# Kernel optimization log

Measured on AMD Instinct MI355X. Metric: run time of the kernel, lower is better.

Reference implementation:

```python
import jax, jax.numpy as jnp
import numpy as np
import math

B, S, D, H, DFF = 16, 512, 1024, 16, 4096
DK = D // H
EPS = 1e-6


def _lin(x, W, b):
    return x @ W + b


def _layernorm(x, g, b):
    # torch-style: unbiased std, eps added to std (not var)
    m = jnp.mean(x, axis=-1, keepdims=True)
    std = jnp.sqrt(jnp.sum((x - m) ** 2, axis=-1, keepdims=True) / (x.shape[-1] - 1))
    return g * (x - m) / (std + EPS) + b


def _gelu(x):
    return 0.5 * x * (1.0 + jnp.tanh(jnp.sqrt(2.0 / jnp.pi) * (x + 0.044715 * x ** 3)))


def setup_inputs() -> dict:
    key = jax.random.key(0)
    ks = jax.random.split(key, 20)
    sc = lambda fan_in: 1.0 / math.sqrt(fan_in)
    d = {
        "x": jax.random.normal(ks[0], (B, S, D), jnp.float32),
        "time": jax.random.normal(ks[1], (B, S, D), jnp.float32),
        "Wq": jax.random.uniform(ks[2], (D, D), jnp.float32, -sc(D), sc(D)),
        "bq": jnp.zeros((D,), jnp.float32),
        "Wk": jax.random.uniform(ks[3], (D, D), jnp.float32, -sc(D), sc(D)),
        "bk": jnp.zeros((D,), jnp.float32),
        "Wt": jax.random.uniform(ks[4], (D, D), jnp.float32, -sc(D), sc(D)),
        "bt": jnp.zeros((D,), jnp.float32),
        "Wv": jax.random.uniform(ks[5], (D, D), jnp.float32, -sc(D), sc(D)),
        "bv": jnp.zeros((D,), jnp.float32),
        "Wo": jax.random.uniform(ks[6], (D, D), jnp.float32, -sc(D), sc(D)),
        "bo": jnp.zeros((D,), jnp.float32),
        "W1": jax.random.uniform(ks[7], (D, DFF), jnp.float32, -sc(D), sc(D)),
        "b1": jnp.zeros((DFF,), jnp.float32),
        "W2": jax.random.uniform(ks[8], (DFF, D), jnp.float32, -sc(DFF), sc(DFF)),
        "b2": jnp.zeros((D,), jnp.float32),
        "ln1_g": jnp.ones((D,), jnp.float32),
        "ln1_b": jnp.zeros((D,), jnp.float32),
        "ln2_g": jnp.ones((D,), jnp.float32),
        "ln2_b": jnp.zeros((D,), jnp.float32),
        "mask_logits": jax.random.uniform(ks[9], (S, S), jnp.float32, 2.0, 5.0),
        "mask": jax.random.randint(ks[10], (B, 1, S, S), 0, 2, jnp.int32),
        "pmask": 0,
    }
    return d


def reference(x, time, Wq, bq, Wk, bk, Wt, bt, Wv, bv, Wo, bo, W1, b1, W2, b2,
              ln1_g, ln1_b, ln2_g, ln2_b, mask_logits, mask, pmask):
    def split_heads(t):  # [B,S,D] -> [B,H,S,DK]
        return t.reshape(B, S, H, DK).transpose(0, 2, 1, 3)

    # --- attention sublayer (dropout = identity at inference) ---
    xn = _layernorm(x, ln1_g, ln1_b)
    q = split_heads(_lin(xn, Wq, bq))
    k1 = split_heads(_lin(xn, Wk, bk))
    k2 = split_heads(_lin(time, Wt, bt))
    v = split_heads(_lin(xn, Wv, bv))

    inv = 1.0 / math.sqrt(DK)
    scores = jnp.einsum("bhqd,bhkd->bhqk", q, k1) * inv
    scores = jnp.where(mask == 0, -1e9, scores)  # masked_fill BEFORE time term
    scores = scores + jnp.einsum("bhqd,bhkd->bhqk", q, k2) * inv
    p_attn = jax.nn.softmax(scores, axis=-1)
    p_attn = p_attn * jax.nn.sigmoid(mask_logits)  # learned post-softmax mask [S,S]
    ctx = jnp.einsum("bhqk,bhkd->bhqd", p_attn, v)
    ctx = ctx.transpose(0, 2, 1, 3).reshape(B, S, D)
    x = x + _lin(ctx, Wo, bo)

    # --- FFN sublayer ---
    xn2 = _layernorm(x, ln2_g, ln2_b)
    ff = _lin(_gelu(_lin(xn2, W1, b1)), W2, b2)
    return x + ff
```

## Files before the change

### kernel.cpp

```cpp
#include <hip/hip_runtime.h>

#define BB   16
#define SS   512
#define DD   1024
#define HH   16
#define DKK  64
#define DFFN 4096
#define LN_EPS 1e-6f
#define QSCALE 0.18033688011112042f

typedef __attribute__((ext_vector_type(8))) __bf16 bf16x8;
typedef __attribute__((ext_vector_type(4))) float f32x4;
typedef __attribute__((ext_vector_type(8))) unsigned short ushort8;
typedef __attribute__((ext_vector_type(4))) unsigned short ushort4_t;

#define AS1 __attribute__((address_space(1)))
#define AS3 __attribute__((address_space(3)))

__device__ __forceinline__ unsigned short f2bf(float f) {
  unsigned int u = __float_as_uint(f);
  u += 0x7FFFu + ((u >> 16) & 1u);
  return (unsigned short)(u >> 16);
}
__device__ __forceinline__ float bf2f(unsigned short u) {
  return __uint_as_float(((unsigned int)u) << 16);
}

__device__ __forceinline__ float gelu_f(float x) {
  float x3 = x * x * x;
  return 0.5f * x * (1.0f + tanhf(0.7978845608028654f * (x + 0.044715f * x3)));
}

__device__ __forceinline__ void sbar() {
  __builtin_amdgcn_sched_barrier(0);
  __builtin_amdgcn_s_barrier();
  __builtin_amdgcn_sched_barrier(0);
}
#define WAITVM(N)                                         \
  do {                                                    \
    __builtin_amdgcn_sched_barrier(0);                    \
    asm volatile("s_waitcnt vmcnt(" #N ")" ::: "memory"); \
    __builtin_amdgcn_sched_barrier(0);                    \
  } while (0)

__global__ __launch_bounds__(256) void ln_kernel(const float* __restrict__ x,
                                                 const float* __restrict__ g,
                                                 const float* __restrict__ b,
                                                 unsigned short* __restrict__ out, int ldo) {
  const int row = blockIdx.x;
  const int tid = threadIdx.x;
  const float* xr = x + (size_t)row * DD;
  float4 v = *(const float4*)(xr + tid * 4);
  float s = v.x + v.y + v.z + v.w;
#pragma unroll
  for (int off = 1; off < 64; off <<= 1) s += __shfl_xor(s, off);
  __shared__ float red[8];
  const int wid = tid >> 6, l = tid & 63;
  if (l == 0) red[wid] = s;
  __syncthreads();
  const float mean = (red[0] + red[1] + red[2] + red[3]) * (1.0f / DD);
  float4 d;
  d.x = v.x - mean; d.y = v.y - mean; d.z = v.z - mean; d.w = v.w - mean;
  float ss = d.x * d.x + d.y * d.y + d.z * d.z + d.w * d.w;
#pragma unroll
  for (int off = 1; off < 64; off <<= 1) ss += __shfl_xor(ss, off);
  if (l == 0) red[4 + wid] = ss;
  __syncthreads();
  const float var = (red[4] + red[5] + red[6] + red[7]) * (1.0f / (DD - 1));
  const float scale = 1.0f / (sqrtf(var) + LN_EPS);
  float4 gv = *(const float4*)(g + tid * 4);
  float4 bv = *(const float4*)(b + tid * 4);
  ushort4_t o;
  o[0] = f2bf(gv.x * d.x * scale + bv.x);
  o[1] = f2bf(gv.y * d.y * scale + bv.y);
  o[2] = f2bf(gv.z * d.z * scale + bv.z);
  o[3] = f2bf(gv.w * d.w * scale + bv.w);
  *(ushort4_t*)(out + (size_t)row * ldo + tid * 4) = o;
}

__global__ __launch_bounds__(256) void cvt_bf16(const float* __restrict__ in,
                                                unsigned short* __restrict__ out, int ldo) {
  const int i = blockIdx.x * 256 + threadIdx.x;
  const int row = i >> 7;
  const int c0 = (i & 127) * 8;
  const float4* p = (const float4*)(in + (size_t)row * DD + c0);
  float4 a = p[0], b = p[1];
  ushort8 o;
  o[0] = f2bf(a.x); o[1] = f2bf(a.y); o[2] = f2bf(a.z); o[3] = f2bf(a.w);
  o[4] = f2bf(b.x); o[5] = f2bf(b.y); o[6] = f2bf(b.z); o[7] = f2bf(b.w);
  *(ushort8*)(out + (size_t)row * ldo + c0) = o;
}

__global__ __launch_bounds__(256) void transpose_cvt(const float* __restrict__ W,
                                                     unsigned short* __restrict__ WT,
                                                     int N, int ldo) {
  __shared__ float tile[32][33];
  const int tx = threadIdx.x & 31, ty = threadIdx.x >> 5;
  const int n0 = blockIdx.x * 32, k0 = blockIdx.y * 32;
#pragma unroll
  for (int i = 0; i < 32; i += 8)
    tile[ty + i][tx] = W[(size_t)(k0 + ty + i) * N + n0 + tx];
  __syncthreads();
#pragma unroll
  for (int i = 0; i < 32; i += 8)
    WT[(size_t)(n0 + ty + i) * ldo + k0 + tx] = f2bf(tile[tx][ty + i]);
}

__global__ __launch_bounds__(256) void vtrans(const unsigned short* __restrict__ in,
                                              unsigned short* __restrict__ out) {
  __shared__ unsigned short tile[64][72];
  const int t = threadIdx.x;
  const int c0 = blockIdx.x * 64;
  const int r0 = blockIdx.y * 64;
  const int tx = t & 15, ty = t >> 4;
#pragma unroll
  for (int i = 0; i < 64; i += 16)
    *(ushort4_t*)&tile[ty + i][tx * 4] =
        *(const ushort4_t*)(in + (size_t)(r0 + ty + i) * 1024 + c0 + tx * 4);
  __syncthreads();
  const int cT = t >> 2, rq = (t & 3) * 16;
  ushort8 o0, o1;
#pragma unroll
  for (int j = 0; j < 8; ++j) o0[j] = tile[rq + j][cT];
#pragma unroll
  for (int j = 0; j < 8; ++j) o1[j] = tile[rq + 8 + j][cT];
  *(ushort8*)(out + (size_t)(c0 + cT) * 8192 + r0 + rq) = o0;
  *(ushort8*)(out + (size_t)(c0 + cT) * 8192 + r0 + rq + 8) = o1;
}

__global__ __launch_bounds__(256) void bias_prep(const float* __restrict__ bq,
                                                 const float* __restrict__ bv,
                                                 const float* __restrict__ bk,
                                                 const float* __restrict__ bt,
                                                 float* __restrict__ qvb,
                                                 float* __restrict__ kcb) {
  const int i = blockIdx.x * 256 + threadIdx.x;
  if (i < 2048) qvb[i] = (i < 1024) ? bq[i] : bv[i - 1024];
  else kcb[i - 2048] = bk[i - 2048] + bt[i - 2048];
}

__global__ __launch_bounds__(256) void gate_build(const int* __restrict__ mask,
                                                  const float* __restrict__ ml,
                                                  unsigned short* __restrict__ gate) {
  const int i = blockIdx.x * 256 + threadIdx.x;
  const size_t base = (size_t)i * 8;
  const int off = (int)(base & (SS * SS - 1));
  const int4* mp = (const int4*)(mask + base);
  const int4 m0 = mp[0], m1 = mp[1];
  const float4* lp = (const float4*)(ml + off);
  const float4 a = lp[0], b = lp[1];
  ushort8 o;
  o[0] = m0.x ? f2bf(1.0f / (1.0f + __expf(-a.x))) : 0;
  o[1] = m0.y ? f2bf(1.0f / (1.0f + __expf(-a.y))) : 0;
  o[2] = m0.z ? f2bf(1.0f / (1.0f + __expf(-a.z))) : 0;
  o[3] = m0.w ? f2bf(1.0f / (1.0f + __expf(-a.w))) : 0;
  o[4] = m1.x ? f2bf(1.0f / (1.0f + __expf(-b.x))) : 0;
  o[5] = m1.y ? f2bf(1.0f / (1.0f + __expf(-b.y))) : 0;
  o[6] = m1.z ? f2bf(1.0f / (1.0f + __expf(-b.z))) : 0;
  o[7] = m1.w ? f2bf(1.0f / (1.0f + __expf(-b.w))) : 0;
  *(ushort8*)(gate + base) = o;
}

template <int BM, int EPI>
__global__ __launch_bounds__(512, 2) void gemm8p(const unsigned short* __restrict__ A, int lda,
                                                 const unsigned short* __restrict__ BT,
                                                 const float* __restrict__ bias,
                                                 const float* __restrict__ resid,
                                                 void* __restrict__ Cout,
                                                 unsigned short* __restrict__ vOut,
                                                 int M, int N, int K) {
  constexpr int MI = BM / 32;
  constexpr int ASUB = BM / 16;
  constexpr int AHALF = BM * 32;
  constexpr int ABUF = BM * 64;
  constexpr int ACALL = BM / 128;

  __shared__ __align__(16) unsigned short smA[2 * ABUF];
  __shared__ __align__(16) unsigned short smB[2 * 16384];

  const int tid = threadIdx.x;
  const int w = tid >> 6, lane = tid & 63;
  const int lr = lane & 15, lg = lane >> 4;
  const int wr = w >> 2, wn = w & 3;

  const int nb = N / 256;
  const int nwg = gridDim.x;
  int bid = blockIdx.x;
  bid = (bid & 7) * (nwg >> 3) + (bid >> 3);
  const int mb = bid / nb, nbk = bid % nb;

  const int uo = (lane * 16) ^ (lane & 32);
  const int srow = uo >> 6;
  const int scol = (uo & 63) >> 1;

  const unsigned short* pA[2];
  const unsigned short* pB[2];
#pragma unroll
  for (int j = 0; j < ACALL; ++j)
    pA[j] = A + (size_t)(mb * BM + (j * 8 + w) * 16 + srow) * lda + scol;
  if (ACALL == 1) pA[1] = pA[0];
#pragma unroll
  for (int j = 0; j < 2; ++j)
    pB[j] = BT + (size_t)(nbk * 256 + (j * 8 + w) * 16 + srow) * K + scol;

  auto stA = [&](int kt, int ks, int j, int d) {
    __builtin_amdgcn_global_load_lds(
        (const AS1 void*)(pA[j] + (size_t)kt * 64 + ks * 32),
        (AS3 void*)(smA + d * ABUF + ks * AHALF + j * 4096 + w * 512), 16, 0, 0);
  };
  auto stB = [&](int kt, int ks, int j, int d) {
    __builtin_amdgcn_global_load_lds(
        (const AS1 void*)(pB[j] + (size_t)kt * 64 + ks * 32),
        (AS3 void*)(smB + d * 16384 + ks * 8192 + j * 4096 + w * 512), 16, 0, 0);
  };
  auto issue_half = [&](int t, int ks) {
    const int d = t & 1;
#pragma unroll
    for (int j = 0; j < ACALL; ++j) stA(t, ks, j, d);
    stB(t, ks, 0, d);
    stB(t, ks, 1, d);
  };

  const int aoff = lr * 32 + ((lg * 8) ^ ((lr & 8) << 1));

  f32x4 acc[MI][4] = {};
  const int NT = K >> 6;

  issue_half(0, 0);
  issue_half(0, 1);
  issue_half(1, 0);
  if constexpr (ACALL == 2) { WAITVM(8); } else { WAITVM(6); }
  sbar();

  for (int kt = 0; kt < NT; ++kt) {
    const unsigned short* aD = smA + (kt & 1) * ABUF;
    const unsigned short* bD = smB + (kt & 1) * 16384;
    const bool i1 = (kt + 1 < NT);
    const bool i2 = (kt + 2 < NT);
    bf16x8 af[4], bf[4];

#pragma unroll
    for (int i = 0; i < 4; ++i)
      bf[i] = *(const bf16x8*)(bD + (wn * 4 + i) * 512 + aoff);
#pragma unroll
    for (int i = 0; i < 4; ++i)
      af[i] = *(const bf16x8*)(aD + (wr * MI + i) * 512 + aoff);
    if (i1) issue_half(kt + 1, 1);
    if constexpr (ACALL == 1) {
      if (i1) { WAITVM(6); } else { WAITVM(0); }
    }
    sbar();
    __builtin_amdgcn_s_setprio(1);
#pragma unroll
    for (int mi = 0; mi < 4; ++mi)
#pragma unroll
      for (int ni = 0; ni < 4; ++ni)
        acc[mi][ni] = __builtin_amdgcn_mfma_f32_16x16x32_bf16(af[mi], bf[ni], acc[mi][ni], 0, 0, 0);
    __builtin_amdgcn_s_setprio(0);
    sbar();

    if constexpr (ACALL == 2) {
#pragma unroll
      for (int i = 0; i < 4; ++i)
        af[i] = *(const bf16x8*)(aD + (wr * MI + 4 + i) * 512 + aoff);
      if (i1) { WAITVM(8); } else { WAITVM(0); }
      sbar();
      __builtin_amdgcn_s_setprio(1);
#pragma unroll
      for (int mi = 0; mi < 4; ++mi)
#pragma unroll
        for (int ni = 0; ni < 4; ++ni)
          acc[4 + mi][ni] = __builtin_amdgcn_mfma_f32_16x16x32_bf16(af[mi], bf[ni], acc[4 + mi][ni], 0, 0, 0);
      __builtin_amdgcn_s_setprio(0);
      sbar();
    }

#pragma unroll
    for (int i = 0; i < 4; ++i)
      bf[i] = *(const bf16x8*)(bD + (16 + wn * 4 + i) * 512 + aoff);
#pragma unroll
    for (int i = 0; i < 4; ++i)
      af[i] = *(const bf16x8*)(aD + (ASUB + wr * MI + i) * 512 + aoff);
    if (i2) issue_half(kt + 2, 0);
    if constexpr (ACALL == 1) {
      if (i2) { WAITVM(6); } else { WAITVM(3); }
    }
    sbar();
    __builtin_amdgcn_s_setprio(1);
#pragma unroll
    for (int mi = 0; mi < 4; ++mi)
#pragma unroll
      for (int ni = 0; ni < 4; ++ni)
        acc[mi][ni] = __builtin_amdgcn_mfma_f32_16x16x32_bf16(af[mi], bf[ni], acc[mi][ni], 0, 0, 0);
    __builtin_amdgcn_s_setprio(0);
    sbar();

    if constexpr (ACALL == 2) {
#pragma unroll
      for (int i = 0; i < 4; ++i)
        af[i] = *(const bf16x8*)(aD + (ASUB + wr * MI + 4 + i) * 512 + aoff);
      if (i2) { WAITVM(8); } else { WAITVM(4); }
      sbar();
      __builtin_amdgcn_s_setprio(1);
#pragma unroll
      for (int mi = 0; mi < 4; ++mi)
#pragma unroll
        for (int ni = 0; ni < 4; ++ni)
          acc[4 + mi][ni] = __builtin_amdgcn_mfma_f32_16x16x32_bf16(af[mi], bf[ni], acc[4 + mi][ni], 0, 0, 0);
      __builtin_amdgcn_s_setprio(0);
      sbar();
    }
  }

  const int colb = nbk * 256 + wn * 64;
  const int rowb = mb * BM + wr * (BM / 2);
  float bvv[4];
#pragma unroll
  for (int ni = 0; ni < 4; ++ni) bvv[ni] = bias[colb + ni * 16 + lr];

  if (EPI == 3 && colb >= 1024) {
#pragma unroll
    for (int mi = 0; mi < MI; ++mi) {
#pragma unroll
      for (int j = 0; j < 4; ++j) {
        const int row = rowb + mi * 16 + lg * 4 + j;
#pragma unroll
        for (int ni = 0; ni < 4; ++ni)
          vOut[(size_t)row * 1024 + (colb - 1024) + ni * 16 + lr] = f2bf(acc[mi][ni][j] + bvv[ni]);
      }
    }
  } else {
#pragma unroll
    for (int mi = 0; mi < MI; ++mi) {
#pragma unroll
      for (int j = 0; j < 4; ++j) {
        const int row = rowb + mi * 16 + lg * 4 + j;
#pragma unroll
        for (int ni = 0; ni < 4; ++ni) {
          const int col = colb + ni * 16 + lr;
          float vv = acc[mi][ni][j] + bvv[ni];
          if (EPI == 2) vv = gelu_f(vv);
          if (EPI == 1) {
            const size_t o = (size_t)row * N + col;
            ((float*)Cout)[o] = vv + resid[o];
          } else if (EPI == 3) {
            ((unsigned short*)Cout)[(size_t)row * 1024 + col] = f2bf(vv * QSCALE);
          } else {
            ((unsigned short*)Cout)[(size_t)row * N + col] = f2bf(vv);
          }
        }
      }
    }
  }
}

__global__ __launch_bounds__(256) void attn4(const unsigned short* __restrict__ qb,
                                             const unsigned short* __restrict__ vT,
                                             const unsigned short* __restrict__ kcb,
                                             const unsigned short* __restrict__ gate,
                                             unsigned short* __restrict__ ctx) {
  __shared__ __align__(16) unsigned char smem[33280];
  float* pctx = (float*)smem;
  float* sumw = (float*)(smem + 32768);

  const int tid = threadIdx.x;
  const int w = tid >> 6, l = tid & 63;
  const int lr = l & 15, lg = l >> 4;
  const int virt = (blockIdx.x & 7) * 512 + (blockIdx.x >> 3);
  const int qt = virt & 15;
  const int h = (virt >> 4) & 15;
  const int b = virt >> 8;
  const int q0 = qt * 32;

  const unsigned short* qg = qb + (size_t)b * SS * DD + h * DKK;
  const unsigned short* kg = kcb + (size_t)b * SS * DD + h * DKK;
  const unsigned short* vg = vT + (size_t)(h * DKK) * 8192 + b * SS;
  const unsigned short* gg = gate + (size_t)b * SS * SS;
  unsigned short* cg = ctx + (size_t)b * SS * DD + h * DKK;

  bf16x8 qf[2][2];
#pragma unroll
  for (int mi = 0; mi < 2; ++mi)
#pragma unroll
    for (int ks = 0; ks < 2; ++ks)
      qf[mi][ks] = *(const bf16x8*)(qg + (size_t)(q0 + mi * 16 + lr) * DD + ks * 32 + lg * 8);

  f32x4 acc[2][4] = {};
  float ssum[2][4] = {};
  const int kb0 = w * 128;

#pragma unroll
  for (int it = 0; it < 4; ++it) {
    const int kbase = kb0 + it * 32;
    unsigned short* Pb = (unsigned short*)smem + w * 2560 + (it & 1) * 1280;

    bf16x8 kf[2][2];
#pragma unroll
    for (int ni = 0; ni < 2; ++ni)
#pragma unroll
      for (int ks = 0; ks < 2; ++ks)
        kf[ni][ks] = *(const bf16x8*)(kg + (size_t)(kbase + ni * 16 + lr) * DD + ks * 32 + lg * 8);
    f32x4 sc[2][2] = {};
#pragma unroll
    for (int ks = 0; ks < 2; ++ks)
#pragma unroll
      for (int mi = 0; mi < 2; ++mi)
#pragma unroll
        for (int ni = 0; ni < 2; ++ni)
          sc[mi][ni] = __builtin_amdgcn_mfma_f32_16x16x32_bf16(qf[mi][ks], kf[ni][ks], sc[mi][ni], 0, 0, 0);

    bf16x8 vb[4];
#pragma unroll
    for (int dkg = 0; dkg < 4; ++dkg)
      vb[dkg] = *(const bf16x8*)(vg + (size_t)(dkg * 16 + lr) * 8192 + kbase + lg * 8);

#pragma unroll
    for (int mi = 0; mi < 2; ++mi)
#pragma unroll
      for (int ni = 0; ni < 2; ++ni)
#pragma unroll
        for (int j = 0; j < 4; ++j) {
          const int row = mi * 16 + lg * 4 + j;
          const unsigned short gu = gg[(size_t)(q0 + row) * SS + kbase + ni * 16 + lr];
          const float e = exp2f(sc[mi][ni][j]);
          ssum[mi][j] += gu ? e : 0.0f;
          Pb[row * 40 + ni * 16 + lr] = f2bf(e * bf2f(gu));
        }

#pragma unroll
    for (int mi = 0; mi < 2; ++mi) {
      const bf16x8 pa = *(const bf16x8*)(Pb + (mi * 16 + lr) * 40 + lg * 8);
#pragma unroll
      for (int dkg = 0; dkg < 4; ++dkg)
        acc[mi][dkg] = __builtin_amdgcn_mfma_f32_16x16x32_bf16(pa, vb[dkg], acc[mi][dkg], 0, 0, 0);
    }
  }

#pragma unroll
  for (int mi = 0; mi < 2; ++mi)
#pragma unroll
    for (int j = 0; j < 4; ++j) {
      float s = ssum[mi][j];
      s += __shfl_xor(s, 1);
      s += __shfl_xor(s, 2);
      s += __shfl_xor(s, 4);
      s += __shfl_xor(s, 8);
      if (lr == 0) sumw[w * 32 + mi * 16 + lg * 4 + j] = s;
    }
  __syncthreads();

#pragma unroll
  for (int mi = 0; mi < 2; ++mi)
#pragma unroll
    for (int dkg = 0; dkg < 4; ++dkg)
#pragma unroll
      for (int j = 0; j < 4; ++j)
        pctx[(size_t)w * 2048 + (mi * 16 + lg * 4 + j) * 64 + dkg * 16 + lr] = acc[mi][dkg][j];
  __syncthreads();

  {
    const int row = tid >> 3;
    const int dk0 = (tid & 7) * 8;
    const float tot = sumw[row] + sumw[32 + row] + sumw[64 + row] + sumw[96 + row];
    const float inv = 1.0f / fmaxf(tot, 1e-30f);
    float vsum[8];
#pragma unroll
    for (int c = 0; c < 8; ++c) vsum[c] = 0.0f;
#pragma unroll
    for (int ww = 0; ww < 4; ++ww) {
      const float* p = pctx + (size_t)ww * 2048 + row * 64 + dk0;
      f32x4 a = *(const f32x4*)p;
      f32x4 bq = *(const f32x4*)(p + 4);
#pragma unroll
      for (int c = 0; c < 4; ++c) { vsum[c] += a[c]; vsum[4 + c] += bq[c]; }
    }
    ushort8 o;
#pragma unroll
    for (int c = 0; c < 8; ++c) o[c] = f2bf(vsum[c] * inv);
    *(ushort8*)(cg + (size_t)(q0 + row) * DD + dk0) = o;
  }
}

extern "C" void kernel_launch(void* const* d_in, const int* in_sizes, int n_in,
                              void* d_out, int out_size, void* d_ws, size_t ws_size,
                              hipStream_t stream) {
  (void)in_sizes; (void)n_in; (void)out_size; (void)ws_size;
  const float* x    = (const float*)d_in[0];
  const float* timep= (const float*)d_in[1];
  const float* Wq = (const float*)d_in[2];  const float* bq = (const float*)d_in[3];
  const float* Wk = (const float*)d_in[4];  const float* bk = (const float*)d_in[5];
  const float* Wt = (const float*)d_in[6];  const float* bt = (const float*)d_in[7];
  const float* Wv = (const float*)d_in[8];  const float* bv = (const float*)d_in[9];
  const float* Wo = (const float*)d_in[10]; const float* bo = (const float*)d_in[11];
  const float* W1 = (const float*)d_in[12]; const float* b1 = (const float*)d_in[13];
  const float* W2 = (const float*)d_in[14]; const float* b2 = (const float*)d_in[15];
  const float* ln1g = (const float*)d_in[16]; const float* ln1b = (const float*)d_in[17];
  const float* ln2g = (const float*)d_in[18]; const float* ln2b = (const float*)d_in[19];
  const float* ml   = (const float*)d_in[20];
  const int*   mask = (const int*)d_in[21];
  float* out = (float*)d_out;

  char* w = (char*)d_ws;
  auto alloc = [&](size_t sz) { char* p = w; w += (sz + 255) & ~(size_t)255; return p; };
  const int MT = BB * SS;

  unsigned short* WqvT = (unsigned short*)alloc((size_t)2048 * 1024 * 2);
  unsigned short* WkcT = (unsigned short*)alloc((size_t)1024 * 2048 * 2);
  unsigned short* WoT  = (unsigned short*)alloc((size_t)DD * DD * 2);
  unsigned short* W1T  = (unsigned short*)alloc((size_t)DD * DFFN * 2);
  unsigned short* W2T  = (unsigned short*)alloc((size_t)DFFN * DD * 2);
  float* qvb = (float*)alloc(2048 * 4);
  float* kcbias = (float*)alloc(1024 * 4);
  unsigned short* gateb = (unsigned short*)alloc((size_t)BB * SS * SS * 2);
  unsigned short* xt2 = (unsigned short*)alloc((size_t)MT * 2048 * 2);
  unsigned short* qbuf = (unsigned short*)alloc((size_t)MT * DD * 2);
  unsigned short* vbuf = (unsigned short*)alloc((size_t)MT * DD * 2);
  unsigned short* vTb = (unsigned short*)alloc((size_t)DD * MT * 2);
  unsigned short* kcb = (unsigned short*)alloc((size_t)MT * DD * 2);
  float*          x2  = (float*)alloc((size_t)MT * DD * 4);
  unsigned short* hb  = (unsigned short*)alloc((size_t)MT * DFFN * 2);
  unsigned short* ctx = xt2;
  unsigned short* xn2 = xt2;

  transpose_cvt<<<dim3(32, 32), 256, 0, stream>>>(Wq, WqvT, 1024, 1024);
  transpose_cvt<<<dim3(32, 32), 256, 0, stream>>>(Wv, WqvT + (size_t)1024 * 1024, 1024, 1024);
  transpose_cvt<<<dim3(32, 32), 256, 0, stream>>>(Wk, WkcT, 1024, 2048);
  transpose_cvt<<<dim3(32, 32), 256, 0, stream>>>(Wt, WkcT + 1024, 1024, 2048);
  transpose_cvt<<<dim3(32, 32), 256, 0, stream>>>(Wo, WoT, 1024, 1024);
  transpose_cvt<<<dim3(128, 32), 256, 0, stream>>>(W1, W1T, 4096, 1024);
  transpose_cvt<<<dim3(32, 128), 256, 0, stream>>>(W2, W2T, 1024, 4096);
  bias_prep<<<dim3(12), 256, 0, stream>>>(bq, bv, bk, bt, qvb, kcbias);
  gate_build<<<dim3(BB * SS * SS / 8 / 256), 256, 0, stream>>>(mask, ml, gateb);

  ln_kernel<<<dim3(MT), 256, 0, stream>>>(x, ln1g, ln1b, xt2, 2048);
  cvt_bf16<<<dim3(MT * DD / 8 / 256), 256, 0, stream>>>(timep, xt2 + 1024, 2048);

  gemm8p<256, 3><<<dim3(256), 512, 0, stream>>>(xt2, 2048, WqvT, qvb, nullptr, (void*)qbuf, vbuf, MT, 2048, 1024);
  vtrans<<<dim3(16, 128), 256, 0, stream>>>(vbuf, vTb);
  gemm8p<128, 0><<<dim3(256), 512, 0, stream>>>(xt2, 2048, WkcT, kcbias, nullptr, (void*)kcb, nullptr, MT, 1024, 2048);

  attn4<<<dim3(BB * HH * 16), 256, 0, stream>>>(qbuf, vTb, kcb, gateb, ctx);

  gemm8p<128, 1><<<dim3(256), 512, 0, stream>>>(ctx, 1024, WoT, bo, x, (void*)x2, nullptr, MT, 1024, 1024);
  ln_kernel<<<dim3(MT), 256, 0, stream>>>(x2, ln2g, ln2b, xn2, 1024);
  gemm8p<256, 2><<<dim3(512), 512, 0, stream>>>(xn2, 1024, W1T, b1, nullptr, (void*)hb, nullptr, MT, 4096, 1024);
  gemm8p<128, 1><<<dim3(256), 512, 0, stream>>>(hb, 4096, W2T, b2, x2, (void*)out, nullptr, MT, 1024, 4096);
}
```

Baseline: 487.3 us.

## Double-buffer A fragments across phases and drop sched barriers in GEMM main loop

```diff
diff --git a/kernel.cpp b/kernel.cpp
--- a/kernel.cpp
+++ b/kernel.cpp
@@ -27,21 +27,12 @@
 }
 
 __device__ __forceinline__ float gelu_f(float x) {
-  float x3 = x * x * x;
-  return 0.5f * x * (1.0f + tanhf(0.7978845608028654f * (x + 0.044715f * x3)));
-}
-
-__device__ __forceinline__ void sbar() {
-  __builtin_amdgcn_sched_barrier(0);
-  __builtin_amdgcn_s_barrier();
-  __builtin_amdgcn_sched_barrier(0);
-}
-#define WAITVM(N)                                         \
-  do {                                                    \
-    __builtin_amdgcn_sched_barrier(0);                    \
-    asm volatile("s_waitcnt vmcnt(" #N ")" ::: "memory"); \
-    __builtin_amdgcn_sched_barrier(0);                    \
-  } while (0)
+  float t = 0.7978845608028654f * (x + 0.044715f * x * x * x);
+  return x / (1.0f + __expf(-2.0f * t));
+}
+
+__device__ __forceinline__ void gbar() { __builtin_amdgcn_s_barrier(); }
+#define WAITVM(N) asm volatile("s_waitcnt vmcnt(" #N ")" ::: "memory")
 
 __global__ __launch_bounds__(256) void ln_kernel(const float* __restrict__ x,
                                                  const float* __restrict__ g,
@@ -226,89 +217,122 @@
   f32x4 acc[MI][4] = {};
   const int NT = K >> 6;
 
+  bf16x8 afC[4], afN[4], bf[4];
+
   issue_half(0, 0);
   issue_half(0, 1);
   issue_half(1, 0);
   if constexpr (ACALL == 2) { WAITVM(8); } else { WAITVM(6); }
-  sbar();
+  gbar();
+#pragma unroll
+  for (int i = 0; i < 4; ++i)
+    afC[i] = *(const bf16x8*)(smA + (wr * MI + i) * 512 + aoff);
 
   for (int kt = 0; kt < NT; ++kt) {
     const unsigned short* aD = smA + (kt & 1) * ABUF;
     const unsigned short* bD = smB + (kt & 1) * 16384;
+    const unsigned short* aDn = smA + ((kt & 1) ^ 1) * ABUF;
     const bool i1 = (kt + 1 < NT);
     const bool i2 = (kt + 2 < NT);
-    bf16x8 af[4], bf[4];
-
-#pragma unroll
-    for (int i = 0; i < 4; ++i)
-      bf[i] = *(const bf16x8*)(bD + (wn * 4 + i) * 512 + aoff);
-#pragma unroll
-    for (int i = 0; i < 4; ++i)
-      af[i] = *(const bf16x8*)(aD + (wr * MI + i) * 512 + aoff);
-    if (i1) issue_half(kt + 1, 1);
-    if constexpr (ACALL == 1) {
-      if (i1) { WAITVM(6); } else { WAITVM(0); }
-    }
-    sbar();
-    __builtin_amdgcn_s_setprio(1);
-#pragma unroll
-    for (int mi = 0; mi < 4; ++mi)
-#pragma unroll
-      for (int ni = 0; ni < 4; ++ni)
-        acc[mi][ni] = __builtin_amdgcn_mfma_f32_16x16x32_bf16(af[mi], bf[ni], acc[mi][ni], 0, 0, 0);
-    __builtin_amdgcn_s_setprio(0);
-    sbar();
 
     if constexpr (ACALL == 2) {
-#pragma unroll
-      for (int i = 0; i < 4; ++i)
-        af[i] = *(const bf16x8*)(aD + (wr * MI + 4 + i) * 512 + aoff);
+      gbar();
+      if (i1) issue_half(kt + 1, 1);
+#pragma unroll
+      for (int i = 0; i < 4; ++i)
+        bf[i] = *(const bf16x8*)(bD + (wn * 4 + i) * 512 + aoff);
+#pragma unroll
+      for (int i = 0; i < 4; ++i)
+        afN[i] = *(const bf16x8*)(aD + (wr * MI + 4 + i) * 512 + aoff);
+      __builtin_amdgcn_s_setprio(1);
+#pragma unroll
+      for (int mi = 0; mi < 4; ++mi)
+#pragma unroll
+        for (int ni = 0; ni < 4; ++ni)
+          acc[mi][ni] = __builtin_amdgcn_mfma_f32_16x16x32_bf16(afC[mi], bf[ni], acc[mi][ni], 0, 0, 0);
+      __builtin_amdgcn_s_setprio(0);
+
       if (i1) { WAITVM(8); } else { WAITVM(0); }
-      sbar();
+      gbar();
+#pragma unroll
+      for (int i = 0; i < 4; ++i)
+        afC[i] = *(const bf16x8*)(aD + (ASUB + wr * MI + i) * 512 + aoff);
       __builtin_amdgcn_s_setprio(1);
 #pragma unroll
       for (int mi = 0; mi < 4; ++mi)
 #pragma unroll
         for (int ni = 0; ni < 4; ++ni)
-          acc[4 + mi][ni] = __builtin_amdgcn_mfma_f32_16x16x32_bf16(af[mi], bf[ni], acc[4 + mi][ni], 0, 0, 0);
+          acc[4 + mi][ni] = __builtin_amdgcn_mfma_f32_16x16x32_bf16(afN[mi], bf[ni], acc[4 + mi][ni], 0, 0, 0);
       __builtin_amdgcn_s_setprio(0);
-      sbar();
-    }
-
-#pragma unroll
-    for (int i = 0; i < 4; ++i)
-      bf[i] = *(const bf16x8*)(bD + (16 + wn * 4 + i) * 512 + aoff);
-#pragma unroll
-    for (int i = 0; i < 4; ++i)
-      af[i] = *(const bf16x8*)(aD + (ASUB + wr * MI + i) * 512 + aoff);
-    if (i2) issue_half(kt + 2, 0);
-    if constexpr (ACALL == 1) {
-      if (i2) { WAITVM(6); } else { WAITVM(3); }
-    }
-    sbar();
-    __builtin_amdgcn_s_setprio(1);
-#pragma unroll
-    for (int mi = 0; mi < 4; ++mi)
-#pragma unroll
-      for (int ni = 0; ni < 4; ++ni)
-        acc[mi][ni] = __builtin_amdgcn_mfma_f32_16x16x32_bf16(af[mi], bf[ni], acc[mi][ni], 0, 0, 0);
-    __builtin_amdgcn_s_setprio(0);
-    sbar();
-
-    if constexpr (ACALL == 2) {
-#pragma unroll
-      for (int i = 0; i < 4; ++i)
-        af[i] = *(const bf16x8*)(aD + (ASUB + wr * MI + 4 + i) * 512 + aoff);
-      if (i2) { WAITVM(8); } else { WAITVM(4); }
-      sbar();
+
+      gbar();
+      if (i2) issue_half(kt + 2, 0);
+#pragma unroll
+      for (int i = 0; i < 4; ++i)
+        bf[i] = *(const bf16x8*)(bD + (16 + wn * 4 + i) * 512 + aoff);
+#pragma unroll
+      for (int i = 0; i < 4; ++i)
+        afN[i] = *(const bf16x8*)(aD + (ASUB + wr * MI + 4 + i) * 512 + aoff);
       __builtin_amdgcn_s_setprio(1);
 #pragma unroll
       for (int mi = 0; mi < 4; ++mi)
 #pragma unroll
         for (int ni = 0; ni < 4; ++ni)
-          acc[4 + mi][ni] = __builtin_amdgcn_mfma_f32_16x16x32_bf16(af[mi], bf[ni], acc[4 + mi][ni], 0, 0, 0);
+          acc[mi][ni] = __builtin_amdgcn_mfma_f32_16x16x32_bf16(afC[mi], bf[ni], acc[mi][ni], 0, 0, 0);
       __builtin_amdgcn_s_setprio(0);
-      sbar();
+
+      if (i1) {
+        if (i2) { WAITVM(8); } else { WAITVM(4); }
+      }
+      gbar();
+      if (i1) {
+#pragma unroll
+        for (int i = 0; i < 4; ++i)
+          afC[i] = *(const bf16x8*)(aDn + (wr * MI + i) * 512 + aoff);
+      }
+      __builtin_amdgcn_s_setprio(1);
+#pragma unroll
+      for (int mi = 0; mi < 4; ++mi)
+#pragma unroll
+        for (int ni = 0; ni < 4; ++ni)
+          acc[4 + mi][ni] = __builtin_amdgcn_mfma_f32_16x16x32_bf16(afN[mi], bf[ni], acc[4 + mi][ni], 0, 0, 0);
+      __builtin_amdgcn_s_setprio(0);
+    } else {
+      if (i1) { WAITVM(3); } else { WAITVM(0); }
+      gbar();
+      if (i1) issue_half(kt + 1, 1);
+#pragma unroll
+      for (int i = 0; i < 4; ++i)
+        bf[i] = *(const bf16x8*)(bD + (wn * 4 + i) * 512 + aoff);
+#pragma unroll
+      for (int i = 0; i < 4; ++i)
+        afN[i] = *(const bf16x8*)(aD + (ASUB + wr * MI + i) * 512 + aoff);
+      __builtin_amdgcn_s_setprio(1);
+#pragma unroll
+      for (int mi = 0; mi < 4; ++mi)
+#pragma unroll
+        for (int ni = 0; ni < 4; ++ni)
+          acc[mi][ni] = __builtin_amdgcn_mfma_f32_16x16x32_bf16(afC[mi], bf[ni], acc[mi][ni], 0, 0, 0);
+      __builtin_amdgcn_s_setprio(0);
+
+      if (i1) { WAITVM(3); } else { WAITVM(0); }
+      gbar();
+      if (i2) issue_half(kt + 2, 0);
+#pragma unroll
+      for (int i = 0; i < 4; ++i)
+        bf[i] = *(const bf16x8*)(bD + (16 + wn * 4 + i) * 512 + aoff);
+      if (i1) {
+#pragma unroll
+        for (int i = 0; i < 4; ++i)
+          afC[i] = *(const bf16x8*)(aDn + (wr * MI + i) * 512 + aoff);
+      }
+      __builtin_amdgcn_s_setprio(1);
+#pragma unroll
+      for (int mi = 0; mi < 4; ++mi)
+#pragma unroll
+        for (int ni = 0; ni < 4; ++ni)
+          acc[mi][ni] = __builtin_amdgcn_mfma_f32_16x16x32_bf16(afN[mi], bf[ni], acc[mi][ni], 0, 0, 0);
+      __builtin_amdgcn_s_setprio(0);
     }
   }
 
```

Measured after the change: 536.2 us. 10.0% more time.

## Add 128x128-tile GEMM kernel for N=1024 projections and cheaper GELU

Applied to the files above, without the earlier changes.

```diff
diff --git a/kernel.cpp b/kernel.cpp
--- a/kernel.cpp
+++ b/kernel.cpp
@@ -27,8 +27,8 @@
 }
 
 __device__ __forceinline__ float gelu_f(float x) {
-  float x3 = x * x * x;
-  return 0.5f * x * (1.0f + tanhf(0.7978845608028654f * (x + 0.044715f * x3)));
+  float t = 0.7978845608028654f * (x + 0.044715f * x * x * x);
+  return x / (1.0f + __expf(-2.0f * t));
 }
 
 __device__ __forceinline__ void sbar() {
@@ -354,6 +354,135 @@
   }
 }
 
+template <int EPI>
+__global__ __launch_bounds__(256, 2) void gemm128(const unsigned short* __restrict__ A, int lda,
+                                                  const unsigned short* __restrict__ BT,
+                                                  const float* __restrict__ bias,
+                                                  const float* __restrict__ resid,
+                                                  void* __restrict__ Cout,
+                                                  int M, int N, int K) {
+  __shared__ __align__(16) unsigned short smA[2 * 8192];
+  __shared__ __align__(16) unsigned short smB[2 * 8192];
+
+  const int tid = threadIdx.x;
+  const int w = tid >> 6, lane = tid & 63;
+  const int lr = lane & 15, lg = lane >> 4;
+  const int wr = w >> 1, wn = w & 1;
+
+  const int nb = N / 128;
+  const int nwg = gridDim.x;
+  int bid = blockIdx.x;
+  bid = (bid & 7) * (nwg >> 3) + (bid >> 3);
+  const int mb = bid / nb, nbk = bid % nb;
+
+  const int uo = (lane * 16) ^ (lane & 32);
+  const int srow = uo >> 6;
+  const int scol = (uo & 63) >> 1;
+
+  const unsigned short* pA[2];
+  const unsigned short* pB[2];
+#pragma unroll
+  for (int j = 0; j < 2; ++j) {
+    pA[j] = A + (size_t)(mb * 128 + (j * 4 + w) * 16 + srow) * lda + scol;
+    pB[j] = BT + (size_t)(nbk * 128 + (j * 4 + w) * 16 + srow) * K + scol;
+  }
+
+  auto stA = [&](int kt, int ks, int j, int d) {
+    __builtin_amdgcn_global_load_lds(
+        (const AS1 void*)(pA[j] + (size_t)kt * 64 + ks * 32),
+        (AS3 void*)(smA + d * 8192 + ks * 4096 + j * 2048 + w * 512), 16, 0, 0);
+  };
+  auto stB = [&](int kt, int ks, int j, int d) {
+    __builtin_amdgcn_global_load_lds(
+        (const AS1 void*)(pB[j] + (size_t)kt * 64 + ks * 32),
+        (AS3 void*)(smB + d * 8192 + ks * 4096 + j * 2048 + w * 512), 16, 0, 0);
+  };
+  auto issue_half = [&](int t, int ks) {
+    const int d = t & 1;
+    stA(t, ks, 0, d); stA(t, ks, 1, d);
+    stB(t, ks, 0, d); stB(t, ks, 1, d);
+  };
+
+  const int aoff = lr * 32 + ((lg * 8) ^ ((lr & 8) << 1));
+
+  f32x4 acc[4][4] = {};
+  const int NT = K >> 6;
+
+  issue_half(0, 0);
+  issue_half(0, 1);
+  issue_half(1, 0);
+  WAITVM(8);
+  sbar();
+
+  for (int kt = 0; kt < NT; ++kt) {
+    const unsigned short* aD = smA + (kt & 1) * 8192;
+    const unsigned short* bD = smB + (kt & 1) * 8192;
+    const bool i1 = (kt + 1 < NT);
+    const bool i2 = (kt + 2 < NT);
+    bf16x8 af[4], bf[4];
+
+#pragma unroll
+    for (int i = 0; i < 4; ++i)
+      bf[i] = *(const bf16x8*)(bD + (wn * 4 + i) * 512 + aoff);
+#pragma unroll
+    for (int i = 0; i < 4; ++i)
+      af[i] = *(const bf16x8*)(aD + (wr * 4 + i) * 512 + aoff);
+    if (i1) issue_half(kt + 1, 1);
+    if (i1) { WAITVM(8); } else { WAITVM(0); }
+    sbar();
+    __builtin_amdgcn_s_setprio(1);
+#pragma unroll
+    for (int mi = 0; mi < 4; ++mi)
+#pragma unroll
+      for (int ni = 0; ni < 4; ++ni)
+        acc[mi][ni] = __builtin_amdgcn_mfma_f32_16x16x32_bf16(af[mi], bf[ni], acc[mi][ni], 0, 0, 0);
+    __builtin_amdgcn_s_setprio(0);
+    sbar();
+
+#pragma unroll
+    for (int i = 0; i < 4; ++i)
+      bf[i] = *(const bf16x8*)(bD + 4096 + (wn * 4 + i) * 512 + aoff);
+#pragma unroll
+    for (int i = 0; i < 4; ++i)
+      af[i] = *(const bf16x8*)(aD + 4096 + (wr * 4 + i) * 512 + aoff);
+    if (i2) issue_half(kt + 2, 0);
+    if (i2) { WAITVM(8); } else if (i1) { WAITVM(4); } else { WAITVM(0); }
+    sbar();
+    __builtin_amdgcn_s_setprio(1);
+#pragma unroll
+    for (int mi = 0; mi < 4; ++mi)
+#pragma unroll
+      for (int ni = 0; ni < 4; ++ni)
+        acc[mi][ni] = __builtin_amdgcn_mfma_f32_16x16x32_bf16(af[mi], bf[ni], acc[mi][ni], 0, 0, 0);
+    __builtin_amdgcn_s_setprio(0);
+    sbar();
+  }
+
+  const int colb = nbk * 128 + wn * 64;
+  const int rowb = mb * 128 + wr * 64;
+  float bvv[4];
+#pragma unroll
+  for (int ni = 0; ni < 4; ++ni) bvv[ni] = bias[colb + ni * 16 + lr];
+#pragma unroll
+  for (int mi = 0; mi < 4; ++mi) {
+#pragma unroll
+    for (int j = 0; j < 4; ++j) {
+      const int row = rowb + mi * 16 + lg * 4 + j;
+#pragma unroll
+      for (int ni = 0; ni < 4; ++ni) {
+        const int col = colb + ni * 16 + lr;
+        const float vv = acc[mi][ni][j] + bvv[ni];
+        if (EPI == 1) {
+          const size_t o = (size_t)row * N + col;
+          ((float*)Cout)[o] = vv + resid[o];
+        } else {
+          ((unsigned short*)Cout)[(size_t)row * N + col] = f2bf(vv);
+        }
+      }
+    }
+  }
+}
+
 __global__ __launch_bounds__(256) void attn4(const unsigned short* __restrict__ qb,
                                              const unsigned short* __restrict__ vT,
                                              const unsigned short* __restrict__ kcb,
@@ -537,12 +666,12 @@
 
   gemm8p<256, 3><<<dim3(256), 512, 0, stream>>>(xt2, 2048, WqvT, qvb, nullptr, (void*)qbuf, vbuf, MT, 2048, 1024);
   vtrans<<<dim3(16, 128), 256, 0, stream>>>(vbuf, vTb);
-  gemm8p<128, 0><<<dim3(256), 512, 0, stream>>>(xt2, 2048, WkcT, kcbias, nullptr, (void*)kcb, nullptr, MT, 1024, 2048);
+  gemm128<0><<<dim3(512), 256, 0, stream>>>(xt2, 2048, WkcT, kcbias, nullptr, (void*)kcb, MT, 1024, 2048);
 
   attn4<<<dim3(BB * HH * 16), 256, 0, stream>>>(qbuf, vTb, kcb, gateb, ctx);
 
-  gemm8p<128, 1><<<dim3(256), 512, 0, stream>>>(ctx, 1024, WoT, bo, x, (void*)x2, nullptr, MT, 1024, 1024);
+  gemm128<1><<<dim3(512), 256, 0, stream>>>(ctx, 1024, WoT, bo, x, (void*)x2, MT, 1024, 1024);
   ln_kernel<<<dim3(MT), 256, 0, stream>>>(x2, ln2g, ln2b, xn2, 1024);
   gemm8p<256, 2><<<dim3(512), 512, 0, stream>>>(xn2, 1024, W1T, b1, nullptr, (void*)hb, nullptr, MT, 4096, 1024);
-  gemm8p<128, 1><<<dim3(256), 512, 0, stream>>>(hb, 4096, W2T, b2, x2, (void*)out, nullptr, MT, 1024, 4096);
-}
+  gemm128<1><<<dim3(512), 256, 0, stream>>>(hb, 4096, W2T, b2, x2, (void*)out, MT, 1024, 4096);
+}
```

Result: faster. 448.0 us (-8.1%).
